# Kernel tuning notes

Measured on AMD Instinct MI355X. Metric: run time of the kernel, lower is better.

Reference implementation:

```python
import jax, jax.numpy as jnp
import numpy as np

RATE = 0.1
INPUT_SHAPE = [8192]
BATCH_DIMS = 1
K = max(1, round(RATE * int(np.prod(INPUT_SHAPE))))  # 819


def setup_inputs() -> dict:
    key = jax.random.key(0)
    x = jax.random.normal(key, (4096, 8192), dtype=jnp.float32)
    return {"x": x}


def reference(x) -> jnp.ndarray:
    batch_flat = int(np.prod(x.shape[:BATCH_DIMS]))
    x_flat = x.reshape(batch_flat, -1)            # [B, D]
    ax = jnp.abs(x_flat)
    topk_vals, _ = jax.lax.top_k(ax, K)           # [B, K] sorted descending
    thr = topk_vals[:, -1:]                        # kth largest |x| per row
    mask = (ax >= thr).reshape(x.shape)
    return jnp.where(mask, x, jnp.zeros_like(x))
```

## Files before the change

### kernel.cpp

```cpp
#include <hip/hip_runtime.h>
#include <stdint.h>


constexpr int NCOLS = 8192;
constexpr int TPB   = 256;
constexpr int V4    = NCOLS / 4;
constexpr int VPT   = V4 / TPB;

constexpr int PAD = 8;
constexpr int W1  = 1024;
constexpr int S1  = W1 + PAD;
constexpr int C1  = 2;
constexpr int B2  = 1024;
constexpr int S2  = B2 + PAD;
constexpr int HW  = (C1 * S1 > S2) ? C1 * S1 : S2;

struct Shared {
  uint32_t hist[HW];
  uint32_t wavesum[4];
  uint32_t digit;
  uint32_t rem;
};

template <int BPT>
__device__ __forceinline__ uint32_t pick_winner(Shared& sh, const uint32_t (&hb)[BPT],
                                                uint32_t& rem, int tid, int lane, int wave) {
  uint32_t L = 0;
#pragma unroll
  for (int j = 0; j < BPT; ++j) L += hb[j];

  uint32_t suf = L;
#pragma unroll
  for (int off = 1; off < 64; off <<= 1) {
    uint32_t o = __shfl_down(suf, off, 64);
    suf += (lane + off < 64) ? o : 0u;
  }
  if (lane == 0) sh.wavesum[wave] = suf;
  __syncthreads();
  uint32_t addw = 0;
#pragma unroll
  for (int w = 0; w < 4; ++w) addw += (w > wave) ? sh.wavesum[w] : 0u;
  suf += addw;

  uint32_t s = suf - L;
#pragma unroll
  for (int j = BPT - 1; j >= 0; --j) {
    uint32_t snext = s;
    s += hb[j];
    if (s >= rem && snext < rem) {
      sh.digit = (uint32_t)(tid * BPT + j);
      sh.rem = rem - snext;
    }
  }
  __syncthreads();
  uint32_t d = sh.digit;
  rem = sh.rem;
  return d;
}

__device__ __forceinline__ uint32_t phase1(Shared& sh, const uint4 (&v)[VPT],
                                           uint32_t& rem, int tid, int lane, int wave) {
  uint4* hz = (uint4*)sh.hist;
  constexpr int ZW4 = (C1 * S1) / 4;
  for (int i = tid; i < ZW4; i += TPB) hz[i] = make_uint4(0u, 0u, 0u, 0u);
  __syncthreads();

  uint32_t* h = &sh.hist[(wave >> 1) * S1];
#pragma unroll
  for (int i = 0; i < VPT; ++i) {
    uint32_t a[4] = {v[i].x, v[i].y, v[i].z, v[i].w};
#pragma unroll
    for (int j = 0; j < 4; ++j) {
      uint32_t d = (a[j] & 0x7fffffffu) >> 20;
      atomicAdd(&h[d & (W1 - 1)], 1u << ((d >> 10) << 4));
    }
  }
  __syncthreads();

  constexpr int BPT = 2048 / TPB;
  uint32_t hb[BPT];
#pragma unroll
  for (int j = 0; j < BPT; ++j) hb[j] = 0;
  const int wbase = (tid & 127) * BPT;
  const int shift = (tid >> 7) << 4;
#pragma unroll
  for (int c = 0; c < C1; ++c) {
    const uint4* hp = (const uint4*)&sh.hist[c * S1 + wbase];
#pragma unroll
    for (int q = 0; q < BPT / 4; ++q) {
      uint4 t = hp[q];
      hb[4 * q + 0] += (t.x >> shift) & 0xffffu;
      hb[4 * q + 1] += (t.y >> shift) & 0xffffu;
      hb[4 * q + 2] += (t.z >> shift) & 0xffffu;
      hb[4 * q + 3] += (t.w >> shift) & 0xffffu;
    }
  }
  return pick_winner<BPT>(sh, hb, rem, tid, lane, wave);
}

__device__ __forceinline__ uint32_t phase23(Shared& sh, const uint4 (&v)[VPT],
                                            int dshift, int cshift, uint32_t cprefix,
                                            uint32_t& rem, int tid, int lane, int wave) {
  uint4* hz = (uint4*)sh.hist;
  constexpr int ZW4 = S2 / 4;
  for (int i = tid; i < ZW4; i += TPB) hz[i] = make_uint4(0u, 0u, 0u, 0u);
  __syncthreads();

#pragma unroll
  for (int i = 0; i < VPT; ++i) {
    uint32_t a[4] = {v[i].x, v[i].y, v[i].z, v[i].w};
#pragma unroll
    for (int j = 0; j < 4; ++j) {
      uint32_t key = a[j] & 0x7fffffffu;
      if ((key >> cshift) == cprefix)
        atomicAdd(&sh.hist[(key >> dshift) & (B2 - 1)], 1u);
    }
  }
  __syncthreads();

  constexpr int BPT = B2 / TPB;
  uint32_t hb[BPT];
  const uint4 t = *(const uint4*)&sh.hist[tid * BPT];
  hb[0] = t.x; hb[1] = t.y; hb[2] = t.z; hb[3] = t.w;
  return pick_winner<BPT>(sh, hb, rem, tid, lane, wave);
}

__global__ __launch_bounds__(TPB, 8) void topk_row_kernel(const float* __restrict__ x,
                                                          float* __restrict__ out,
                                                          int K) {
  __shared__ Shared sh;
  const int row  = blockIdx.x;
  const int tid  = threadIdx.x;
  const int lane = tid & 63;
  const int wave = tid >> 6;

  const uint4* xr = (const uint4*)(x) + (size_t)row * V4;
  uint4 v[VPT];
#pragma unroll
  for (int i = 0; i < VPT; ++i) v[i] = xr[tid + i * TPB];

  uint32_t rem = (uint32_t)K;
  uint32_t d1 = phase1(sh, v, rem, tid, lane, wave);
  uint32_t d2 = phase23(sh, v, 10, 20, d1, rem, tid, lane, wave);
  uint32_t d3 = phase23(sh, v,  0, 10, (d1 << 10) | d2, rem, tid, lane, wave);

  const uint32_t thr = (d1 << 20) | (d2 << 10) | d3;

  uint4* outr = (uint4*)(out) + (size_t)row * V4;
#pragma unroll
  for (int i = 0; i < VPT; ++i) {
    uint4 o = v[i];
    o.x = ((o.x & 0x7fffffffu) >= thr) ? o.x : 0u;
    o.y = ((o.y & 0x7fffffffu) >= thr) ? o.y : 0u;
    o.z = ((o.z & 0x7fffffffu) >= thr) ? o.z : 0u;
    o.w = ((o.w & 0x7fffffffu) >= thr) ? o.w : 0u;
    outr[tid + i * TPB] = o;
  }
}

extern "C" void kernel_launch(void* const* d_in, const int* in_sizes, int n_in,
                              void* d_out, int out_size, void* d_ws, size_t ws_size,
                              hipStream_t stream) {
  (void)n_in; (void)out_size; (void)d_ws; (void)ws_size;
  const float* x = (const float*)d_in[0];
  float* out = (float*)d_out;
  const int rows = in_sizes[0] / NCOLS;
  const int K = (int)(0.1 * NCOLS + 0.5);
  topk_row_kernel<<<rows, TPB, 0, stream>>>(x, out, K);
}
```

Before: 230.2 us.

## Process four rows per block with double-buffered register prefetch of next row

Each block now handles four consecutive rows. While one row goes through the three-pass radix histogram selection, the next row is loaded from global memory into a second register buffer. The aim is to hide global load latency behind the shared-memory histogram work. Register use doubles, so launch bounds drop from 8 to 4 blocks per CU and the grid shrinks fourfold, which lowers occupancy and parallelism.

New measurement: 244.3 us. 6.2% more time.

```diff
diff --git a/kernel.cpp b/kernel.cpp
--- a/kernel.cpp
+++ b/kernel.cpp
@@ -6,6 +6,7 @@
 constexpr int TPB   = 256;
 constexpr int V4    = NCOLS / 4;
 constexpr int VPT   = V4 / TPB;
+constexpr int ROWS  = 4;
 
 constexpr int PAD = 8;
 constexpr int W1  = 1024;
@@ -125,28 +126,21 @@
   return pick_winner<BPT>(sh, hb, rem, tid, lane, wave);
 }
 
-__global__ __launch_bounds__(TPB, 8) void topk_row_kernel(const float* __restrict__ x,
-                                                          float* __restrict__ out,
-                                                          int K) {
-  __shared__ Shared sh;
-  const int row  = blockIdx.x;
-  const int tid  = threadIdx.x;
-  const int lane = tid & 63;
-  const int wave = tid >> 6;
-
-  const uint4* xr = (const uint4*)(x) + (size_t)row * V4;
-  uint4 v[VPT];
+__device__ __forceinline__ void load_row(uint4 (&v)[VPT], const uint4* __restrict__ xr,
+                                         int tid) {
 #pragma unroll
   for (int i = 0; i < VPT; ++i) v[i] = xr[tid + i * TPB];
+}
 
+__device__ __forceinline__ void process_row(Shared& sh, const uint4 (&v)[VPT],
+                                            uint4* __restrict__ outr, int K,
+                                            int tid, int lane, int wave) {
   uint32_t rem = (uint32_t)K;
   uint32_t d1 = phase1(sh, v, rem, tid, lane, wave);
   uint32_t d2 = phase23(sh, v, 10, 20, d1, rem, tid, lane, wave);
   uint32_t d3 = phase23(sh, v,  0, 10, (d1 << 10) | d2, rem, tid, lane, wave);
-
   const uint32_t thr = (d1 << 20) | (d2 << 10) | d3;
 
-  uint4* outr = (uint4*)(out) + (size_t)row * V4;
 #pragma unroll
   for (int i = 0; i < VPT; ++i) {
     uint4 o = v[i];
@@ -158,6 +152,37 @@
   }
 }
 
+__global__ __launch_bounds__(TPB, 4) void topk_row_kernel(const float* __restrict__ x,
+                                                          float* __restrict__ out,
+                                                          int K, int nrows) {
+  __shared__ Shared sh;
+  const int tid  = threadIdx.x;
+  const int lane = tid & 63;
+  const int wave = tid >> 6;
+  const int row0 = blockIdx.x * ROWS;
+
+  const uint4* xr   = (const uint4*)(x)  + (size_t)row0 * V4;
+  uint4*       outr = (uint4*)(out)      + (size_t)row0 * V4;
+
+  uint4 va[VPT], vb[VPT];
+  const int nr = nrows - row0;
+
+  load_row(va, xr, tid);
+  if (nr > 1) load_row(vb, xr + V4, tid);
+  process_row(sh, va, outr, K, tid, lane, wave);
+  if (nr > 1) {
+    if (nr > 2) load_row(va, xr + 2 * V4, tid);
+    process_row(sh, vb, outr + V4, K, tid, lane, wave);
+  }
+  if (nr > 2) {
+    if (nr > 3) load_row(vb, xr + 3 * V4, tid);
+    process_row(sh, va, outr + 2 * V4, K, tid, lane, wave);
+  }
+  if (nr > 3) {
+    process_row(sh, vb, outr + 3 * V4, K, tid, lane, wave);
+  }
+}
+
 extern "C" void kernel_launch(void* const* d_in, const int* in_sizes, int n_in,
                               void* d_out, int out_size, void* d_ws, size_t ws_size,
                               hipStream_t stream) {
@@ -166,5 +191,6 @@
   float* out = (float*)d_out;
   const int rows = in_sizes[0] / NCOLS;
   const int K = (int)(0.1 * NCOLS + 0.5);
-  topk_row_kernel<<<rows, TPB, 0, stream>>>(x, out, K);
+  const int grid = (rows + ROWS - 1) / ROWS;
+  topk_row_kernel<<<grid, TPB, 0, stream>>>(x, out, K, rows);
 }
```

## Process multiple rows per block with double-buffered async global-to-LDS prefetch

Applied to the files above, without the earlier changes.

Each block now handles 8 rows and stages them into a two-slot LDS buffer with global_load_lds, prefetching row i+2 while row i is being processed. The histogram phases read from LDS instead of registers. Barriers become manual waitcnt plus s_barrier. This is meant to hide global load latency behind the radix-select work. In exchange, the grid shrinks to 512 blocks and LDS grows to about 72KB per block, so occupancy drops to about two blocks per CU. The vmcnt counting also depends on stores not being counted, which may be fragile.

Result: slower. 244.9 us (+6.4%).

```diff
diff --git a/kernel.cpp b/kernel.cpp
--- a/kernel.cpp
+++ b/kernel.cpp
@@ -6,6 +6,7 @@
 constexpr int TPB   = 256;
 constexpr int V4    = NCOLS / 4;
 constexpr int VPT   = V4 / TPB;
+constexpr int RPB   = 8;
 
 constexpr int PAD = 8;
 constexpr int W1  = 1024;
@@ -16,12 +17,32 @@
 constexpr int HW  = (C1 * S1 > S2) ? C1 * S1 : S2;
 
 struct Shared {
+  uint32_t row[2][NCOLS];
   uint32_t hist[HW];
   uint32_t wavesum[4];
   uint32_t digit;
   uint32_t rem;
 };
 
+__device__ __forceinline__ void lds_barrier() {
+  asm volatile("s_waitcnt lgkmcnt(0)" ::: "memory");
+  __builtin_amdgcn_s_barrier();
+  asm volatile("" ::: "memory");
+}
+
+__device__ __forceinline__ void prefetch_row(const uint32_t* __restrict__ gsrc,
+                                             uint32_t* ldst, int wave, int lane) {
+  const uint32_t* g = gsrc + wave * (NCOLS / 4) + lane * 4;
+  uint32_t* l = ldst + wave * (NCOLS / 4);
+#pragma unroll
+  for (int i = 0; i < 8; ++i) {
+    __builtin_amdgcn_global_load_lds(
+        (const __attribute__((address_space(1))) uint32_t*)(g + i * 256),
+        (__attribute__((address_space(3))) uint32_t*)(l + i * 256),
+        16, 0, 0);
+  }
+}
+
 template <int BPT>
 __device__ __forceinline__ uint32_t pick_winner(Shared& sh, const uint32_t (&hb)[BPT],
                                                 uint32_t& rem, int tid, int lane, int wave) {
@@ -36,7 +57,7 @@
     suf += (lane + off < 64) ? o : 0u;
   }
   if (lane == 0) sh.wavesum[wave] = suf;
-  __syncthreads();
+  lds_barrier();
   uint32_t addw = 0;
 #pragma unroll
   for (int w = 0; w < 4; ++w) addw += (w > wave) ? sh.wavesum[w] : 0u;
@@ -52,30 +73,31 @@
       sh.rem = rem - snext;
     }
   }
-  __syncthreads();
+  lds_barrier();
   uint32_t d = sh.digit;
   rem = sh.rem;
   return d;
 }
 
-__device__ __forceinline__ uint32_t phase1(Shared& sh, const uint4 (&v)[VPT],
+__device__ __forceinline__ uint32_t phase1(Shared& sh, const uint4* __restrict__ rv,
                                            uint32_t& rem, int tid, int lane, int wave) {
   uint4* hz = (uint4*)sh.hist;
   constexpr int ZW4 = (C1 * S1) / 4;
   for (int i = tid; i < ZW4; i += TPB) hz[i] = make_uint4(0u, 0u, 0u, 0u);
-  __syncthreads();
+  lds_barrier();
 
   uint32_t* h = &sh.hist[(wave >> 1) * S1];
 #pragma unroll
   for (int i = 0; i < VPT; ++i) {
-    uint32_t a[4] = {v[i].x, v[i].y, v[i].z, v[i].w};
+    uint4 t = rv[tid + i * TPB];
+    uint32_t a[4] = {t.x, t.y, t.z, t.w};
 #pragma unroll
     for (int j = 0; j < 4; ++j) {
       uint32_t d = (a[j] & 0x7fffffffu) >> 20;
       atomicAdd(&h[d & (W1 - 1)], 1u << ((d >> 10) << 4));
     }
   }
-  __syncthreads();
+  lds_barrier();
 
   constexpr int BPT = 2048 / TPB;
   uint32_t hb[BPT];
@@ -98,17 +120,18 @@
   return pick_winner<BPT>(sh, hb, rem, tid, lane, wave);
 }
 
-__device__ __forceinline__ uint32_t phase23(Shared& sh, const uint4 (&v)[VPT],
+__device__ __forceinline__ uint32_t phase23(Shared& sh, const uint4* __restrict__ rv,
                                             int dshift, int cshift, uint32_t cprefix,
                                             uint32_t& rem, int tid, int lane, int wave) {
   uint4* hz = (uint4*)sh.hist;
   constexpr int ZW4 = S2 / 4;
   for (int i = tid; i < ZW4; i += TPB) hz[i] = make_uint4(0u, 0u, 0u, 0u);
-  __syncthreads();
+  lds_barrier();
 
 #pragma unroll
   for (int i = 0; i < VPT; ++i) {
-    uint32_t a[4] = {v[i].x, v[i].y, v[i].z, v[i].w};
+    uint4 t = rv[tid + i * TPB];
+    uint32_t a[4] = {t.x, t.y, t.z, t.w};
 #pragma unroll
     for (int j = 0; j < 4; ++j) {
       uint32_t key = a[j] & 0x7fffffffu;
@@ -116,7 +139,7 @@
         atomicAdd(&sh.hist[(key >> dshift) & (B2 - 1)], 1u);
     }
   }
-  __syncthreads();
+  lds_barrier();
 
   constexpr int BPT = B2 / TPB;
   uint32_t hb[BPT];
@@ -125,36 +148,63 @@
   return pick_winner<BPT>(sh, hb, rem, tid, lane, wave);
 }
 
-__global__ __launch_bounds__(TPB, 8) void topk_row_kernel(const float* __restrict__ x,
+__global__ __launch_bounds__(TPB, 2) void topk_row_kernel(const float* __restrict__ x,
                                                           float* __restrict__ out,
-                                                          int K) {
+                                                          int K, int nrows) {
   __shared__ Shared sh;
-  const int row  = blockIdx.x;
   const int tid  = threadIdx.x;
   const int lane = tid & 63;
   const int wave = tid >> 6;
-
-  const uint4* xr = (const uint4*)(x) + (size_t)row * V4;
-  uint4 v[VPT];
-#pragma unroll
-  for (int i = 0; i < VPT; ++i) v[i] = xr[tid + i * TPB];
-
-  uint32_t rem = (uint32_t)K;
-  uint32_t d1 = phase1(sh, v, rem, tid, lane, wave);
-  uint32_t d2 = phase23(sh, v, 10, 20, d1, rem, tid, lane, wave);
-  uint32_t d3 = phase23(sh, v,  0, 10, (d1 << 10) | d2, rem, tid, lane, wave);
-
-  const uint32_t thr = (d1 << 20) | (d2 << 10) | d3;
-
-  uint4* outr = (uint4*)(out) + (size_t)row * V4;
-#pragma unroll
-  for (int i = 0; i < VPT; ++i) {
-    uint4 o = v[i];
-    o.x = ((o.x & 0x7fffffffu) >= thr) ? o.x : 0u;
-    o.y = ((o.y & 0x7fffffffu) >= thr) ? o.y : 0u;
-    o.z = ((o.z & 0x7fffffffu) >= thr) ? o.z : 0u;
-    o.w = ((o.w & 0x7fffffffu) >= thr) ? o.w : 0u;
-    outr[tid + i * TPB] = o;
+  const int row0 = blockIdx.x * RPB;
+  if (row0 >= nrows) return;
+  const int R = (nrows - row0 < RPB) ? (nrows - row0) : RPB;
+
+  const uint32_t* xg = (const uint32_t*)x + (size_t)row0 * NCOLS;
+  uint32_t*       og = (uint32_t*)out + (size_t)row0 * NCOLS;
+
+  prefetch_row(xg, sh.row[0], wave, lane);
+  if (R > 1) {
+    prefetch_row(xg + NCOLS, sh.row[1], wave, lane);
+    asm volatile("s_waitcnt vmcnt(8)" ::: "memory");
+  } else {
+    asm volatile("s_waitcnt vmcnt(0)" ::: "memory");
+  }
+  __builtin_amdgcn_s_barrier();
+  asm volatile("" ::: "memory");
+
+  int cur = 0;
+  for (int it = 0; it < R; ++it) {
+    const uint4* rv = (const uint4*)sh.row[cur];
+
+    uint32_t rem = (uint32_t)K;
+    uint32_t d1 = phase1(sh, rv, rem, tid, lane, wave);
+    uint32_t d2 = phase23(sh, rv, 10, 20, d1, rem, tid, lane, wave);
+    uint32_t d3 = phase23(sh, rv, 0, 10, (d1 << 10) | d2, rem, tid, lane, wave);
+    const uint32_t thr = (d1 << 20) | (d2 << 10) | d3;
+
+    uint4* outr = (uint4*)(og + (size_t)it * NCOLS);
+#pragma unroll
+    for (int i = 0; i < VPT; ++i) {
+      uint4 o = rv[tid + i * TPB];
+      o.x = ((o.x & 0x7fffffffu) >= thr) ? o.x : 0u;
+      o.y = ((o.y & 0x7fffffffu) >= thr) ? o.y : 0u;
+      o.z = ((o.z & 0x7fffffffu) >= thr) ? o.z : 0u;
+      o.w = ((o.w & 0x7fffffffu) >= thr) ? o.w : 0u;
+      outr[tid + i * TPB] = o;
+    }
+
+    lds_barrier();
+
+    const bool pf = (it + 2 < R);
+    if (pf) prefetch_row(xg + (size_t)(it + 2) * NCOLS, sh.row[cur], wave, lane);
+
+    if (it + 1 < R) {
+      if (pf) asm volatile("s_waitcnt vmcnt(16)" ::: "memory");
+      else    asm volatile("s_waitcnt vmcnt(8)"  ::: "memory");
+      __builtin_amdgcn_s_barrier();
+      asm volatile("" ::: "memory");
+    }
+    cur ^= 1;
   }
 }
 
@@ -166,5 +216,6 @@
   float* out = (float*)d_out;
   const int rows = in_sizes[0] / NCOLS;
   const int K = (int)(0.1 * NCOLS + 0.5);
-  topk_row_kernel<<<rows, TPB, 0, stream>>>(x, out, K);
-}
+  const int grid = (rows + RPB - 1) / RPB;
+  topk_row_kernel<<<grid, TPB, 0, stream>>>(x, out, K, rows);
+}
```
